# Kernel tuning notes

Hardware: AMD Instinct MI355X
Metric: run time of the kernel (lower is better)

## Reference

```python
import jax, jax.numpy as jnp
import numpy as np

B, S, D, H, E, K = 4, 1024, 1024, 4096, 8, 2

def setup_inputs() -> dict:
    key = jax.random.key(0)
    ks = jax.random.split(key, 6)
    sd = 1.0 / np.sqrt(D)
    sh = 1.0 / np.sqrt(H)
    return {
        "x": jax.random.normal(ks[0], (B, S, D), jnp.float32),
        "Wg": jax.random.normal(ks[1], (D, E), jnp.float32) * sd,
        "bg": jnp.zeros((E,), jnp.float32),
        "W1": jax.random.normal(ks[2], (E, D, H), jnp.float32) * sd,
        "b1": jnp.zeros((E, H), jnp.float32),
        "Wa": jax.random.normal(ks[3], (E, D, H), jnp.float32) * sd,
        "ba": jnp.zeros((E, H), jnp.float32),
        "W2": jax.random.normal(ks[4], (E, H, D), jnp.float32) * sh,
        "b2": jnp.zeros((E, D), jnp.float32),
        "kv_cache": 0,
    }

def reference(x, Wg, bg, W1, b1, Wa, ba, W2, b2, kv_cache):
    # gate: softmax over experts, top-k, renormalize
    gate = jax.nn.softmax(x @ Wg + bg, axis=-1)            # [B,S,E]
    w, idx = jax.lax.top_k(gate, K)                        # [B,S,K]
    w = w / jnp.sum(w, axis=-1, keepdims=True)
    # dense all-expert FF with SwiGLU: fc2( silu(fc_a(x)) * fc1(x) )
    a = jnp.einsum('bsd,edh->bseh', x, Wa) + ba            # [B,S,E,H]
    g = a * jax.nn.sigmoid(a)
    u = jnp.einsum('bsd,edh->bseh', x, W1) + b1
    y = jnp.einsum('bseh,ehd->bsed', g * u, W2) + b2       # [B,S,E,D]
    # gather top-k experts per token and combine
    sel = jnp.take_along_axis(y, idx[..., None], axis=2)   # [B,S,K,D]
    out = jnp.sum(sel * w[..., None], axis=-2)             # [B,S,D]
    return out
```

## Files before the change

### kernel.cpp

```cpp
#include <hip/hip_runtime.h>
#include <hip/hip_bf16.h>
#include <math.h>

#define TOKENS 4096
#define DD 1024
#define HH 4096
#define NE 8
#define PAIRS 8192
#define ROWCAP 8448
#define T1CAP 40
#define TCAP 72
#define G1_NT 32
#define G2_NT 128

typedef __bf16 bf16x8 __attribute__((ext_vector_type(8)));
typedef float f32x4 __attribute__((ext_vector_type(4)));

__device__ __forceinline__ unsigned short f2bf(float f) {
  union { float f; unsigned int u; } c; c.f = f;
  unsigned int x = c.u;
  return (unsigned short)((x + 0x7fffu + ((x >> 16) & 1u)) >> 16);
}

__device__ __forceinline__ void lds16(void* l, const void* g) {
  __builtin_amdgcn_global_load_lds((const __attribute__((address_space(1))) void*)g,
                                   (__attribute__((address_space(3))) void*)l, 16, 0, 0);
}

__global__ void init_kernel(int* counts) {
  if (threadIdx.x < NE) counts[threadIdx.x] = 0;
}

__global__ __launch_bounds__(256) void transpose_kernel(
    const float* __restrict__ Wa, const float* __restrict__ W1, const float* __restrict__ W2,
    unsigned short* __restrict__ WaT, unsigned short* __restrict__ W1T,
    unsigned short* __restrict__ W2T) {
  int b = blockIdx.x;
  int sec = b >> 13;
  int sb = b & 8191;
  const float* in; unsigned short* out; int R, C;
  if (sec == 0)      { in = Wa; out = WaT; R = DD; C = HH; }
  else if (sec == 1) { in = W1; out = W1T; R = DD; C = HH; }
  else               { in = W2; out = W2T; R = HH; C = DD; }
  int ntr = R >> 6, ntc = C >> 6;
  int per_e = ntr * ntc;
  int e = sb / per_e;
  int rem = sb - e * per_e;
  int tr = rem / ntc, tc = rem - (rem / ntc) * ntc;
  const float* ie = in + (size_t)e * R * C;
  unsigned short* oe = out + (size_t)e * R * C;

  __shared__ float t[64][68];
  int tid = threadIdx.x;
  int lr = tid >> 2;
  int c4 = (tid & 3) << 4;
  const float* src = ie + (size_t)(tr * 64 + lr) * C + tc * 64 + c4;
  float4 v0 = *(const float4*)(src);
  float4 v1 = *(const float4*)(src + 4);
  float4 v2 = *(const float4*)(src + 8);
  float4 v3 = *(const float4*)(src + 12);
  *(float4*)&t[lr][c4] = v0;
  *(float4*)&t[lr][c4 + 4] = v1;
  *(float4*)&t[lr][c4 + 8] = v2;
  *(float4*)&t[lr][c4 + 12] = v3;
  __syncthreads();

  int oc = tid >> 2;
  int r0 = (tid & 3) << 4;
  unsigned int pk[8];
#pragma unroll
  for (int i = 0; i < 8; i++) {
    unsigned int lo = f2bf(t[r0 + 2 * i][oc]);
    unsigned int hi = f2bf(t[r0 + 2 * i + 1][oc]);
    pk[i] = lo | (hi << 16);
  }
  unsigned short* dst = oe + (size_t)(tc * 64 + oc) * R + tr * 64 + r0;
  *(uint4*)(dst) = make_uint4(pk[0], pk[1], pk[2], pk[3]);
  *(uint4*)(dst + 8) = make_uint4(pk[4], pk[5], pk[6], pk[7]);
}

__global__ __launch_bounds__(256) void gate_kernel(const float* __restrict__ x,
    const float* __restrict__ Wg, const float* __restrict__ bg,
    int* __restrict__ counts, int* __restrict__ tok_e, int* __restrict__ tok_slot,
    float* __restrict__ tok_w) {
  int t = blockIdx.x, tid = threadIdx.x;
  const float* xr = x + (size_t)t * DD;
  float p[8] = {0, 0, 0, 0, 0, 0, 0, 0};
  for (int d = tid; d < DD; d += 256) {
    float xv = xr[d];
    const float4* wrow = (const float4*)(Wg + (size_t)d * NE);
    float4 w0 = wrow[0], w1 = wrow[1];
    p[0] += xv * w0.x; p[1] += xv * w0.y; p[2] += xv * w0.z; p[3] += xv * w0.w;
    p[4] += xv * w1.x; p[5] += xv * w1.y; p[6] += xv * w1.z; p[7] += xv * w1.w;
  }
#pragma unroll
  for (int e = 0; e < 8; e++) {
    p[e] += __shfl_down(p[e], 32);
    p[e] += __shfl_down(p[e], 16);
    p[e] += __shfl_down(p[e], 8);
    p[e] += __shfl_down(p[e], 4);
    p[e] += __shfl_down(p[e], 2);
    p[e] += __shfl_down(p[e], 1);
  }
  __shared__ float red[4][8];
  if ((tid & 63) == 0) {
#pragma unroll
    for (int e = 0; e < 8; e++) red[tid >> 6][e] = p[e];
  }
  __syncthreads();
  if (tid == 0) {
    float l[8];
#pragma unroll
    for (int e = 0; e < 8; e++) l[e] = red[0][e] + red[1][e] + red[2][e] + red[3][e] + bg[e];
    int e0 = 0; float l0 = l[0];
    for (int e = 1; e < 8; e++) if (l[e] > l0) { e0 = e; l0 = l[e]; }
    int e1 = -1; float l1 = -3.4e38f;
    for (int e = 0; e < 8; e++) if (e != e0 && l[e] > l1) { e1 = e; l1 = l[e]; }
    float w0 = 1.f / (1.f + __expf(l1 - l0));
    float w1 = 1.f - w0;
    int s0 = atomicAdd(&counts[e0], 1);
    int s1 = atomicAdd(&counts[e1], 1);
    tok_e[2 * t] = e0;     tok_slot[2 * t] = s0;     tok_w[2 * t] = w0;
    tok_e[2 * t + 1] = e1; tok_slot[2 * t + 1] = s1; tok_w[2 * t + 1] = w1;
  }
}

__global__ void scan_kernel(const int* __restrict__ counts, int* __restrict__ offsets,
                            int* __restrict__ tm1_e, int* __restrict__ tm1_row0,
                            int* __restrict__ tm1_nrow, int* __restrict__ ntp1,
                            int* __restrict__ tm2_e, int* __restrict__ tm2_row0,
                            int* __restrict__ tm2_nrow, int* __restrict__ ntp2) {
  if (threadIdx.x != 0 || blockIdx.x != 0) return;
  int c[NE];
#pragma unroll
  for (int e = 0; e < NE; e++) c[e] = counts[e];
  int off = 0, n1 = 0, n2 = 0;
  for (int e = 0; e < NE; e++) {
    offsets[e] = off;
    for (int r = 0; r < c[e]; r += 256) {
      tm1_e[n1] = e; tm1_row0[n1] = off + r;
      tm1_nrow[n1] = (c[e] - r < 256) ? (c[e] - r) : 256;
      n1++;
    }
    for (int r = 0; r < c[e]; r += 128) {
      tm2_e[n2] = e; tm2_row0[n2] = off + r;
      tm2_nrow[n2] = (c[e] - r < 128) ? (c[e] - r) : 128;
      n2++;
    }
    off += c[e];
  }
  *ntp1 = n1;
  *ntp2 = n2;
}

__global__ __launch_bounds__(64) void gather_kernel(const float* __restrict__ x,
    const int* __restrict__ tok_e, const int* __restrict__ tok_slot,
    const float* __restrict__ tok_w, const int* __restrict__ offsets,
    unsigned short* __restrict__ Xe, int* __restrict__ pair_row, float* __restrict__ rw) {
  int pp = blockIdx.x, tid = threadIdx.x;
  int e = tok_e[pp];
  int row = offsets[e] + tok_slot[pp];
  int t = pp >> 1;
  const float* src = x + (size_t)t * DD + tid * 16;
  float4 v0 = *(const float4*)(src);
  float4 v1 = *(const float4*)(src + 4);
  float4 v2 = *(const float4*)(src + 8);
  float4 v3 = *(const float4*)(src + 12);
  unsigned int pk[8];
  pk[0] = f2bf(v0.x) | ((unsigned int)f2bf(v0.y) << 16);
  pk[1] = f2bf(v0.z) | ((unsigned int)f2bf(v0.w) << 16);
  pk[2] = f2bf(v1.x) | ((unsigned int)f2bf(v1.y) << 16);
  pk[3] = f2bf(v1.z) | ((unsigned int)f2bf(v1.w) << 16);
  pk[4] = f2bf(v2.x) | ((unsigned int)f2bf(v2.y) << 16);
  pk[5] = f2bf(v2.z) | ((unsigned int)f2bf(v2.w) << 16);
  pk[6] = f2bf(v3.x) | ((unsigned int)f2bf(v3.y) << 16);
  pk[7] = f2bf(v3.z) | ((unsigned int)f2bf(v3.w) << 16);
  unsigned short* dst = Xe + (size_t)row * DD + tid * 16;
  *(uint4*)(dst) = make_uint4(pk[0], pk[1], pk[2], pk[3]);
  *(uint4*)(dst + 8) = make_uint4(pk[4], pk[5], pk[6], pk[7]);
  if (tid == 0) { pair_row[pp] = row; rw[row] = tok_w[pp]; }
}


__global__ __launch_bounds__(512, 2) void gemm1_kernel(
    const unsigned short* __restrict__ Xe,
    const unsigned short* __restrict__ WaT,
    const unsigned short* __restrict__ W1T,
    const float* __restrict__ ba, const float* __restrict__ b1,
    unsigned short* __restrict__ h,
    const int* __restrict__ tm_e, const int* __restrict__ tm_row0,
    const int* __restrict__ tm_nrow, const int* __restrict__ ntp) {
  __shared__ unsigned short sm[2][12288];

  int work = blockIdx.x;
  int tile = work >> 6;
  if (tile >= *ntp) return;
  int n0 = (work & 63) << 6;
  int e = tm_e[tile], row0 = tm_row0[tile], nrow = tm_nrow[tile];

  int tid = threadIdx.x;
  int l = tid & 63, w = tid >> 6;
  int wm = w >> 1, wn = w & 1;
  int fr = l & 15, kc = l >> 4;

  int arow = (w << 4) + (l >> 2);
  int cd = l & 3;
  int swzA = (cd ^ ((arow >> 1) & 3)) << 3;
  const unsigned short* pA1 = Xe + (size_t)(row0 + arow) * DD + swzA;
  const unsigned short* pA2 = pA1 + (size_t)128 * DD;
  int brow = (w < 4) ? arow : (arow - 64);
  int swzB = (cd ^ ((brow >> 1) & 3)) << 3;
  const unsigned short* pB = ((w < 4) ? WaT : W1T) + ((size_t)e << 22) +
                             (size_t)(n0 + brow) * DD + swzB;

  unsigned short* smb = &sm[0][0];
  int dA1 = (w << 10) + (l << 4);
  int dA2 = dA1 + 8192;
  int dB  = 16384 + ((w & 3) << 10) + ((w >= 4) ? 4096 : 0) + (l << 4);

  int aof[4], bof[2];
#pragma unroll
  for (int m = 0; m < 4; m++) {
    int r = wm * 64 + m * 16 + fr;
    aof[m] = r * 64 + ((kc ^ ((r >> 1) & 3)) << 4);
  }
#pragma unroll
  for (int n = 0; n < 2; n++) {
    int r = wn * 32 + n * 16 + fr;
    bof[n] = 16384 + r * 64 + ((kc ^ ((r >> 1) & 3)) << 4);
  }

  f32x4 accA[4][2], accU[4][2];
  f32x4 z = {0.f, 0.f, 0.f, 0.f};
#pragma unroll
  for (int m = 0; m < 4; m++)
#pragma unroll
    for (int n = 0; n < 2; n++) { accA[m][n] = z; accU[m][n] = z; }

  auto stage = [&](int T, int buf) {
    int koff = (T < G1_NT ? T : G1_NT - 1) << 5;
    char* base = (char*)smb + buf * 24576;
    lds16(base + dA1, pA1 + koff);
    lds16(base + dA2, pA2 + koff);
    lds16(base + dB,  pB  + koff);
  };

  stage(0, 0);
  __syncthreads();
  int buf = 0;
  for (int T = 0; T < G1_NT; ++T) {
    stage(T + 1, buf ^ 1);
    const char* lb = (const char*)smb + buf * 24576;
    bf16x8 a[4], bA[2], bU[2];
#pragma unroll
    for (int m = 0; m < 4; m++) a[m] = *(const bf16x8*)(lb + aof[m]);
#pragma unroll
    for (int n = 0; n < 2; n++) {
      bA[n] = *(const bf16x8*)(lb + bof[n]);
      bU[n] = *(const bf16x8*)(lb + bof[n] + 4096);
    }
#pragma unroll
    for (int m = 0; m < 4; m++)
#pragma unroll
      for (int n = 0; n < 2; n++) {
        accA[m][n] = __builtin_amdgcn_mfma_f32_16x16x32_bf16(a[m], bA[n], accA[m][n], 0, 0, 0);
        accU[m][n] = __builtin_amdgcn_mfma_f32_16x16x32_bf16(a[m], bU[n], accU[m][n], 0, 0, 0);
      }
    __syncthreads();
    buf ^= 1;
  }

  int lr4 = kc * 4;
#pragma unroll
  for (int n = 0; n < 2; n++) {
    int col = n0 + wn * 32 + n * 16 + fr;
    float bav = ba[e * HH + col];
    float buv = b1[e * HH + col];
#pragma unroll
    for (int m = 0; m < 4; m++) {
#pragma unroll
      for (int j = 0; j < 4; j++) {
        int r = wm * 64 + m * 16 + lr4 + j;
        if (r < nrow) {
          float av = accA[m][n][j] + bav;
          float uv = accU[m][n][j] + buv;
          float s = __builtin_amdgcn_rcpf(1.f + __expf(-av));
          h[(size_t)(row0 + r) * HH + col] = f2bf(av * s * uv);
        }
      }
    }
  }
}

__global__ __launch_bounds__(512, 2) void gemm2_kernel(
    const unsigned short* __restrict__ hb,
    const unsigned short* __restrict__ W2T,
    const float* __restrict__ b2, const float* __restrict__ rw,
    float* __restrict__ contrib,
    const int* __restrict__ tm_e, const int* __restrict__ tm_row0,
    const int* __restrict__ tm_nrow, const int* __restrict__ ntp) {
  __shared__ unsigned short sm[2][12288];

  int work = blockIdx.x;
  int tile = work >> 2;
  if (tile >= *ntp) return;
  int n0 = (work & 3) << 8;
  int e = tm_e[tile], row0 = tm_row0[tile], nrow = tm_nrow[tile];

  int tid = threadIdx.x;
  int l = tid & 63, w = tid >> 6;
  int wm = w >> 2, wn = w & 3;
  int fr = l & 15, kc = l >> 4;

  int arow = (w << 4) + (l >> 2);
  int cd = l & 3;
  int swzA = (cd ^ ((arow >> 1) & 3)) << 3;
  const unsigned short* pA = hb + (size_t)(row0 + arow) * HH + swzA;
  const unsigned short* pB1 = W2T + ((size_t)e << 22) + (size_t)(n0 + arow) * HH + swzA;
  const unsigned short* pB2 = pB1 + (size_t)128 * HH;

  unsigned short* smb = &sm[0][0];
  int dA  = (w << 10) + (l << 4);
  int dB1 = 8192 + (w << 10) + (l << 4);
  int dB2 = dB1 + 8192;

  int aof[4], bof[4];
#pragma unroll
  for (int m = 0; m < 4; m++) {
    int r = wm * 64 + m * 16 + fr;
    aof[m] = r * 64 + ((kc ^ ((r >> 1) & 3)) << 4);
  }
#pragma unroll
  for (int n = 0; n < 4; n++) {
    int rb = wn * 64 + n * 16 + fr;
    bof[n] = 8192 + rb * 64 + ((kc ^ ((rb >> 1) & 3)) << 4);
  }

  f32x4 acc[4][4];
  f32x4 z = {0.f, 0.f, 0.f, 0.f};
#pragma unroll
  for (int m = 0; m < 4; m++)
#pragma unroll
    for (int n = 0; n < 4; n++) acc[m][n] = z;

  auto stage = [&](int T, int buf) {
    int koff = (T < G2_NT ? T : G2_NT - 1) << 5;
    char* base = (char*)smb + buf * 24576;
    lds16(base + dA,  pA  + koff);
    lds16(base + dB1, pB1 + koff);
    lds16(base + dB2, pB2 + koff);
  };

  stage(0, 0);
  __syncthreads();
  int buf = 0;
  for (int T = 0; T < G2_NT; ++T) {
    stage(T + 1, buf ^ 1);
    const char* lb = (const char*)smb + buf * 24576;
    bf16x8 a[4], b[4];
#pragma unroll
    for (int m = 0; m < 4; m++) a[m] = *(const bf16x8*)(lb + aof[m]);
#pragma unroll
    for (int n = 0; n < 4; n++) b[n] = *(const bf16x8*)(lb + bof[n]);
#pragma unroll
    for (int m = 0; m < 4; m++)
#pragma unroll
      for (int n = 0; n < 4; n++)
        acc[m][n] = __builtin_amdgcn_mfma_f32_16x16x32_bf16(a[m], b[n], acc[m][n], 0, 0, 0);
    __syncthreads();
    buf ^= 1;
  }

  float b2v[4];
#pragma unroll
  for (int n = 0; n < 4; n++) b2v[n] = b2[e * DD + n0 + wn * 64 + n * 16 + fr];
  int lr4 = kc * 4;
#pragma unroll
  for (int m = 0; m < 4; m++) {
#pragma unroll
    for (int j = 0; j < 4; j++) {
      int r = wm * 64 + m * 16 + lr4 + j;
      if (r < nrow) {
        float wv = rw[row0 + r];
        float* dst = contrib + (size_t)(row0 + r) * DD + n0 + wn * 64 + fr;
#pragma unroll
        for (int n = 0; n < 4; n++)
          dst[n * 16] = wv * (acc[m][n][j] + b2v[n]);
      }
    }
  }
}

__global__ __launch_bounds__(256) void combine_kernel(const float* __restrict__ contrib,
    const int* __restrict__ pair_row, float* __restrict__ out) {
  int t = blockIdx.x, tid = threadIdx.x;
  int r0 = pair_row[2 * t], r1 = pair_row[2 * t + 1];
  const float4* c0 = (const float4*)(contrib + (size_t)r0 * DD);
  const float4* c1 = (const float4*)(contrib + (size_t)r1 * DD);
  float4* o = (float4*)(out + (size_t)t * DD);
  float4 a = c0[tid], b = c1[tid];
  o[tid] = make_float4(a.x + b.x, a.y + b.y, a.z + b.z, a.w + b.w);
}

extern "C" void kernel_launch(void* const* d_in, const int* in_sizes, int n_in,
                              void* d_out, int out_size, void* d_ws, size_t ws_size,
                              hipStream_t stream) {
  const float* x  = (const float*)d_in[0];
  const float* Wg = (const float*)d_in[1];
  const float* bg = (const float*)d_in[2];
  const float* W1 = (const float*)d_in[3];
  const float* b1 = (const float*)d_in[4];
  const float* Wa = (const float*)d_in[5];
  const float* ba = (const float*)d_in[6];
  const float* W2 = (const float*)d_in[7];
  const float* b2 = (const float*)d_in[8];
  float* out = (float*)d_out;
  (void)in_sizes; (void)n_in; (void)out_size; (void)ws_size;

  char* p = (char*)d_ws;
  auto take = [&](size_t bytes) { char* r = p; p += (bytes + 255) & ~(size_t)255; return r; };
  unsigned short* WaT = (unsigned short*)take((size_t)NE * HH * DD * 2);
  unsigned short* W1T = (unsigned short*)take((size_t)NE * HH * DD * 2);
  unsigned short* W2T = (unsigned short*)take((size_t)NE * DD * HH * 2);
  unsigned short* Xe  = (unsigned short*)take((size_t)ROWCAP * DD * 2);
  unsigned short* hb  = (unsigned short*)take((size_t)ROWCAP * HH * 2);
  float* contrib      = (float*)take((size_t)ROWCAP * DD * 4);
  int* counts   = (int*)take(64);
  int* offsets  = (int*)take(64);
  int* tok_e    = (int*)take(PAIRS * 4);
  int* tok_slot = (int*)take(PAIRS * 4);
  float* tok_w  = (float*)take(PAIRS * 4);
  int* pair_row = (int*)take(PAIRS * 4);
  float* rw     = (float*)take(ROWCAP * 4);
  int* tm1_e    = (int*)take(T1CAP * 4);
  int* tm1_row0 = (int*)take(T1CAP * 4);
  int* tm1_nrow = (int*)take(T1CAP * 4);
  int* ntp1     = (int*)take(64);
  int* tm2_e    = (int*)take(TCAP * 4);
  int* tm2_row0 = (int*)take(TCAP * 4);
  int* tm2_nrow = (int*)take(TCAP * 4);
  int* ntp2     = (int*)take(64);

  init_kernel<<<1, 64, 0, stream>>>(counts);
  transpose_kernel<<<3 * 8192, 256, 0, stream>>>(Wa, W1, W2, WaT, W1T, W2T);
  gate_kernel<<<TOKENS, 256, 0, stream>>>(x, Wg, bg, counts, tok_e, tok_slot, tok_w);
  scan_kernel<<<1, 64, 0, stream>>>(counts, offsets, tm1_e, tm1_row0, tm1_nrow, ntp1,
                                    tm2_e, tm2_row0, tm2_nrow, ntp2);
  gather_kernel<<<PAIRS, 64, 0, stream>>>(x, tok_e, tok_slot, tok_w, offsets, Xe, pair_row, rw);
  gemm1_kernel<<<T1CAP * 64, 512, 0, stream>>>(Xe, WaT, W1T, ba, b1, hb, tm1_e, tm1_row0, tm1_nrow, ntp1);
  gemm2_kernel<<<TCAP * 4, 512, 0, stream>>>(hb, W2T, b2, rw, contrib, tm2_e, tm2_row0, tm2_nrow, ntp2);
  combine_kernel<<<TOKENS, 256, 0, stream>>>(contrib, pair_row, out);
}
```

Measured before the change: 574.1 us.

## Fuse combine into gemm2 via atomic adds and shrink gemm2 tiles

Measured after the change: 1.480 ms. 158% more time.

```diff
diff --git a/kernel.cpp b/kernel.cpp
--- a/kernel.cpp
+++ b/kernel.cpp
@@ -82,8 +82,9 @@
 __global__ __launch_bounds__(256) void gate_kernel(const float* __restrict__ x,
     const float* __restrict__ Wg, const float* __restrict__ bg,
     int* __restrict__ counts, int* __restrict__ tok_e, int* __restrict__ tok_slot,
-    float* __restrict__ tok_w) {
+    float* __restrict__ tok_w, float* __restrict__ out) {
   int t = blockIdx.x, tid = threadIdx.x;
+  ((float4*)(out + (size_t)t * DD))[tid] = make_float4(0.f, 0.f, 0.f, 0.f);
   const float* xr = x + (size_t)t * DD;
   float p[8] = {0, 0, 0, 0, 0, 0, 0, 0};
   for (int d = tid; d < DD; d += 256) {
@@ -156,7 +157,7 @@
 __global__ __launch_bounds__(64) void gather_kernel(const float* __restrict__ x,
     const int* __restrict__ tok_e, const int* __restrict__ tok_slot,
     const float* __restrict__ tok_w, const int* __restrict__ offsets,
-    unsigned short* __restrict__ Xe, int* __restrict__ pair_row, float* __restrict__ rw) {
+    unsigned short* __restrict__ Xe, int* __restrict__ row2tok, float* __restrict__ rw) {
   int pp = blockIdx.x, tid = threadIdx.x;
   int e = tok_e[pp];
   int row = offsets[e] + tok_slot[pp];
@@ -178,11 +179,11 @@
   unsigned short* dst = Xe + (size_t)row * DD + tid * 16;
   *(uint4*)(dst) = make_uint4(pk[0], pk[1], pk[2], pk[3]);
   *(uint4*)(dst + 8) = make_uint4(pk[4], pk[5], pk[6], pk[7]);
-  if (tid == 0) { pair_row[pp] = row; rw[row] = tok_w[pp]; }
-}
-
-
-__global__ __launch_bounds__(512, 2) void gemm1_kernel(
+  if (tid == 0) { row2tok[row] = t; rw[row] = tok_w[pp]; }
+}
+
+
+__global__ __launch_bounds__(512, 6) void gemm1_kernel(
     const unsigned short* __restrict__ Xe,
     const unsigned short* __restrict__ WaT,
     const unsigned short* __restrict__ W1T,
@@ -292,37 +293,36 @@
   }
 }
 
-__global__ __launch_bounds__(512, 2) void gemm2_kernel(
+__global__ __launch_bounds__(256) void gemm2_kernel(
     const unsigned short* __restrict__ hb,
     const unsigned short* __restrict__ W2T,
     const float* __restrict__ b2, const float* __restrict__ rw,
-    float* __restrict__ contrib,
+    const int* __restrict__ row2tok, float* __restrict__ out,
     const int* __restrict__ tm_e, const int* __restrict__ tm_row0,
     const int* __restrict__ tm_nrow, const int* __restrict__ ntp) {
-  __shared__ unsigned short sm[2][12288];
+  __shared__ unsigned short sm[2][8192];
 
   int work = blockIdx.x;
-  int tile = work >> 2;
+  int tile = work >> 3;
   if (tile >= *ntp) return;
-  int n0 = (work & 3) << 8;
+  int n0 = (work & 7) << 7;
   int e = tm_e[tile], row0 = tm_row0[tile], nrow = tm_nrow[tile];
 
   int tid = threadIdx.x;
-  int l = tid & 63, w = tid >> 6;
-  int wm = w >> 2, wn = w & 3;
-  int fr = l & 15, kc = l >> 4;
-
-  int arow = (w << 4) + (l >> 2);
-  int cd = l & 3;
-  int swzA = (cd ^ ((arow >> 1) & 3)) << 3;
-  const unsigned short* pA = hb + (size_t)(row0 + arow) * HH + swzA;
-  const unsigned short* pB1 = W2T + ((size_t)e << 22) + (size_t)(n0 + arow) * HH + swzA;
-  const unsigned short* pB2 = pB1 + (size_t)128 * HH;
-
-  unsigned short* smb = &sm[0][0];
-  int dA  = (w << 10) + (l << 4);
-  int dB1 = 8192 + (w << 10) + (l << 4);
-  int dB2 = dB1 + 8192;
+  int lane = tid & 63, wid = tid >> 6;
+  int wm = wid >> 1, wn = wid & 1;
+  int fr = lane & 15, kc = lane >> 4;
+
+  int srow = tid >> 2;
+  int cd = tid & 3;
+  int scl = (cd ^ ((srow >> 1) & 3)) << 3;
+
+  const unsigned short* pA0 = hb + (size_t)(row0 + srow) * HH + scl;
+  const unsigned short* pA1 = hb + (size_t)(row0 + 64 + srow) * HH + scl;
+  const unsigned short* pB0 = W2T + ((size_t)e << 22) + (size_t)(n0 + srow) * HH + scl;
+  const unsigned short* pB1 = W2T + ((size_t)e << 22) + (size_t)(n0 + 64 + srow) * HH + scl;
+
+  unsigned short* ldst = &sm[0][0] + (size_t)tid * 8;
 
   int aof[4], bof[4];
 #pragma unroll
@@ -332,8 +332,8 @@
   }
 #pragma unroll
   for (int n = 0; n < 4; n++) {
-    int rb = wn * 64 + n * 16 + fr;
-    bof[n] = 8192 + rb * 64 + ((kc ^ ((rb >> 1) & 3)) << 4);
+    int r = wn * 64 + n * 16 + fr;
+    bof[n] = 8192 + r * 64 + ((kc ^ ((r >> 1) & 3)) << 4);
   }
 
   f32x4 acc[4][4];
@@ -345,10 +345,11 @@
 
   auto stage = [&](int T, int buf) {
     int koff = (T < G2_NT ? T : G2_NT - 1) << 5;
-    char* base = (char*)smb + buf * 24576;
-    lds16(base + dA,  pA  + koff);
-    lds16(base + dB1, pB1 + koff);
-    lds16(base + dB2, pB2 + koff);
+    unsigned short* L = ldst + buf * 8192;
+    lds16(L, pA0 + koff);
+    lds16(L + 2048, pA1 + koff);
+    lds16(L + 4096, pB0 + koff);
+    lds16(L + 6144, pB1 + koff);
   };
 
   stage(0, 0);
@@ -356,7 +357,7 @@
   int buf = 0;
   for (int T = 0; T < G2_NT; ++T) {
     stage(T + 1, buf ^ 1);
-    const char* lb = (const char*)smb + buf * 24576;
+    const char* lb = (const char*)&sm[0][0] + (buf << 14);
     bf16x8 a[4], b[4];
 #pragma unroll
     for (int m = 0; m < 4; m++) a[m] = *(const bf16x8*)(lb + aof[m]);
@@ -381,25 +382,16 @@
     for (int j = 0; j < 4; j++) {
       int r = wm * 64 + m * 16 + lr4 + j;
       if (r < nrow) {
-        float wv = rw[row0 + r];
-        float* dst = contrib + (size_t)(row0 + r) * DD + n0 + wn * 64 + fr;
+        int row = row0 + r;
+        float wv = rw[row];
+        int t = row2tok[row];
+        float* dst = out + (size_t)t * DD + n0 + wn * 64 + fr;
 #pragma unroll
         for (int n = 0; n < 4; n++)
-          dst[n * 16] = wv * (acc[m][n][j] + b2v[n]);
+          atomicAdd(&dst[n * 16], wv * (acc[m][n][j] + b2v[n]));
       }
     }
   }
-}
-
-__global__ __launch_bounds__(256) void combine_kernel(const float* __restrict__ contrib,
-    const int* __restrict__ pair_row, float* __restrict__ out) {
-  int t = blockIdx.x, tid = threadIdx.x;
-  int r0 = pair_row[2 * t], r1 = pair_row[2 * t + 1];
-  const float4* c0 = (const float4*)(contrib + (size_t)r0 * DD);
-  const float4* c1 = (const float4*)(contrib + (size_t)r1 * DD);
-  float4* o = (float4*)(out + (size_t)t * DD);
-  float4 a = c0[tid], b = c1[tid];
-  o[tid] = make_float4(a.x + b.x, a.y + b.y, a.z + b.z, a.w + b.w);
 }
 
 extern "C" void kernel_launch(void* const* d_in, const int* in_sizes, int n_in,
@@ -424,13 +416,12 @@
   unsigned short* W2T = (unsigned short*)take((size_t)NE * DD * HH * 2);
   unsigned short* Xe  = (unsigned short*)take((size_t)ROWCAP * DD * 2);
   unsigned short* hb  = (unsigned short*)take((size_t)ROWCAP * HH * 2);
-  float* contrib      = (float*)take((size_t)ROWCAP * DD * 4);
   int* counts   = (int*)take(64);
   int* offsets  = (int*)take(64);
   int* tok_e    = (int*)take(PAIRS * 4);
   int* tok_slot = (int*)take(PAIRS * 4);
   float* tok_w  = (float*)take(PAIRS * 4);
-  int* pair_row = (int*)take(PAIRS * 4);
+  int* row2tok  = (int*)take(ROWCAP * 4);
   float* rw     = (float*)take(ROWCAP * 4);
   int* tm1_e    = (int*)take(T1CAP * 4);
   int* tm1_row0 = (int*)take(T1CAP * 4);
@@ -443,11 +434,10 @@
 
   init_kernel<<<1, 64, 0, stream>>>(counts);
   transpose_kernel<<<3 * 8192, 256, 0, stream>>>(Wa, W1, W2, WaT, W1T, W2T);
-  gate_kernel<<<TOKENS, 256, 0, stream>>>(x, Wg, bg, counts, tok_e, tok_slot, tok_w);
+  gate_kernel<<<TOKENS, 256, 0, stream>>>(x, Wg, bg, counts, tok_e, tok_slot, tok_w, out);
   scan_kernel<<<1, 64, 0, stream>>>(counts, offsets, tm1_e, tm1_row0, tm1_nrow, ntp1,
                                     tm2_e, tm2_row0, tm2_nrow, ntp2);
-  gather_kernel<<<PAIRS, 64, 0, stream>>>(x, tok_e, tok_slot, tok_w, offsets, Xe, pair_row, rw);
+  gather_kernel<<<PAIRS, 64, 0, stream>>>(x, tok_e, tok_slot, tok_w, offsets, Xe, row2tok, rw);
   gemm1_kernel<<<T1CAP * 64, 512, 0, stream>>>(Xe, WaT, W1T, ba, b1, hb, tm1_e, tm1_row0, tm1_nrow, ntp1);
-  gemm2_kernel<<<TCAP * 4, 512, 0, stream>>>(hb, W2T, b2, rw, contrib, tm2_e, tm2_row0, tm2_nrow, ntp2);
-  combine_kernel<<<TOKENS, 256, 0, stream>>>(contrib, pair_row, out);
-}
+  gemm2_kernel<<<TCAP * 8, 256, 0, stream>>>(hb, W2T, b2, rw, row2tok, out, tm2_e, tm2_row0, tm2_nrow, ntp2);
+}
```
